# Kernel tuning notes

Measured on AMD Instinct MI355X. Metric: run time of the kernel, lower is better.

## Reference

```python
import jax, jax.numpy as jnp
import numpy as np

B, C, NS, NT = 8, 256, 16384, 2048
KQ = 64            # self-attention key/query dim
D = 64             # cond_conv_feat_dim
W0, W1, W2 = D * D, D * D, D * 1   # dynamic weight sizes (predict_mask=True)
B0, B1, B2 = D, D, 1
CTRL = W0 + W1 + W2 + B0 + B1 + B2  # 8385


def setup_inputs() -> dict:
    key = jax.random.key(0)
    ks = jax.random.split(key, 9)
    return {
        "scene_feat": jax.random.normal(ks[0], (B, C, NS), jnp.float32),
        "template_feat": jax.random.normal(ks[1], (B, C, NT), jnp.float32),
        # SelfAttention 1x1-conv (= linear over channels) weights
        "q_w": jax.random.normal(ks[2], (KQ, C), jnp.float32) * 0.02,
        "k_w": jax.random.normal(ks[3], (KQ, C), jnp.float32) * 0.02,
        "v_w": jax.random.normal(ks[4], (C, C), jnp.float32) * 0.02,
        # projection head of SimpleAggregator: Conv1d(3*C -> D, k=1) + ReLU
        "proj_w": jax.random.normal(ks[5], (D, 3 * C), jnp.float32) * 0.02,
        "proj_b": jnp.zeros((D,), jnp.float32),
        # controller head: Linear(C -> CTRL), init normal(std=0.01), bias 0
        "ctrl_w": jax.random.normal(ks[6], (CTRL, C), jnp.float32) * 0.01,
        "ctrl_b": jnp.zeros((CTRL,), jnp.float32),
    }


def _self_attention(x, q_w, k_w, v_w):
    # x: [B, C, N] -> [B, C_out, N]
    q = jnp.einsum("kc,bcn->bnk", q_w, x)          # [B, N, KQ]
    k = jnp.einsum("kc,bcn->bkn", k_w, x)          # [B, KQ, N]
    v = jnp.einsum("oc,bcn->bno", v_w, x)          # [B, N, C_out]
    attn = jax.nn.softmax(jnp.einsum("bnk,bkm->bnm", q / jnp.sqrt(jnp.float32(KQ)), k), axis=-1)
    y = jnp.einsum("bnm,bmo->bon", attn, v)        # [B, C_out, N]
    return y


def reference(scene_feat, template_feat, q_w, k_w, v_w, proj_w, proj_b, ctrl_w, ctrl_b):
    # ---- SimpleAggregator (self-attention on template inside) ----
    t_sa = _self_attention(template_feat, q_w, k_w, v_w)       # [B, C, NT]
    t_max = jnp.max(t_sa, axis=-1, keepdims=True)              # [B, C, 1]
    aggr = jnp.concatenate(
        [scene_feat - t_max, scene_feat * t_max, scene_feat], axis=1
    )                                                          # [B, 3C, NS]
    x = jax.nn.relu(jnp.einsum("oc,bcn->bon", proj_w, aggr) + proj_b[None, :, None])  # [B, D, NS]

    # ---- controller head on ORIGINAL template_feat max-pooled ----
    pooled = jnp.max(template_feat, axis=-1)                   # [B, C]
    params = pooled @ ctrl_w.T + ctrl_b                        # [B, CTRL]

    # parse_dynamic_params: splits = weights then biases
    o = 0
    w0 = params[:, o:o + W0].reshape(B, D, D); o += W0
    w1 = params[:, o:o + W1].reshape(B, D, D); o += W1
    w2 = params[:, o:o + W2].reshape(B, 1, D); o += W2
    b0 = params[:, o:o + B0]; o += B0
    b1 = params[:, o:o + B1]; o += B1
    b2 = params[:, o:o + B2]

    # per-sample dynamic 1x1 convs (groups=batch trick == batched GEMM)
    x = jax.nn.relu(jnp.einsum("boi,bin->bon", w0, x) + b0[:, :, None])
    x = jax.nn.relu(jnp.einsum("boi,bin->bon", w1, x) + b1[:, :, None])
    x = jnp.einsum("boi,bin->bon", w2, x) + b2[:, :, None]    # [B, 1, NS], no relu (mask layer)
    return x.reshape(B, NS)
```

## Files before the change

kernel.cpp:

```cpp
#include <hip/hip_runtime.h>


typedef __attribute__((ext_vector_type(8))) short short8;
typedef __attribute__((ext_vector_type(4))) short short4v;
typedef __attribute__((ext_vector_type(4))) float f32x4;

__device__ __forceinline__ unsigned short f2bf(float f){
  unsigned u = __float_as_uint(f);
  u += 0x7FFFu + ((u >> 16) & 1u);
  return (unsigned short)(u >> 16);
}
__device__ __forceinline__ unsigned fenc(float f){
  unsigned u = __float_as_uint(f);
  return (u & 0x80000000u) ? ~u : (u | 0x80000000u);
}
__device__ __forceinline__ float fdec(unsigned k){
  unsigned u = (k & 0x80000000u) ? (k & 0x7FFFFFFFu) : ~k;
  return __uint_as_float(u);
}

__global__ __launch_bounds__(256) void k0w(const float* __restrict__ qw,
    const float* __restrict__ kw, const float* __restrict__ vw,
    unsigned short* __restrict__ Wbf, unsigned* __restrict__ tmaxe,
    unsigned* __restrict__ pooledEnc){
  if (blockIdx.x == 0){
    const unsigned ninf = fenc(-3.0e38f);
    for (int i = threadIdx.x; i < 2048; i += 256){
      tmaxe[i] = 0u;
      pooledEnc[i] = ninf;
    }
  }
  const int e = (blockIdx.x * 256 + threadIdx.x) * 4;
  const int row = e >> 8, c = e & 255;
  const float* src;
  float scl = 1.0f;
  if (row < 64){ src = qw + row * 256 + c; scl = 0.125f; }
  else if (row < 128){ src = kw + (row - 64) * 256 + c; }
  else { src = vw + (row - 128) * 256 + c; }
  float4 v = *(const float4*)src;
  short4v o;
  o[0] = (short)f2bf(v.x * scl); o[1] = (short)f2bf(v.y * scl);
  o[2] = (short)f2bf(v.z * scl); o[3] = (short)f2bf(v.w * scl);
  *(short4v*)(Wbf + e) = o;
}

__global__ __launch_bounds__(256) void k0_tt(const float* __restrict__ T,
    unsigned short* __restrict__ Tt, unsigned* __restrict__ pooledEnc){
  const int b = blockIdx.x, nt = blockIdx.y, ct = blockIdx.z;
  const int n0 = nt * 128, c0 = ct * 32;
  const int tid = threadIdx.x;
  __shared__ float Ls[32][129];
  const int cr = tid >> 3, nq = tid & 7;
  const float* src = T + ((size_t)b * 256 + c0 + cr) * 2048 + n0 + nq * 16;
  float4 v0 = ((const float4*)src)[0];
  float4 v1 = ((const float4*)src)[1];
  float4 v2 = ((const float4*)src)[2];
  float4 v3 = ((const float4*)src)[3];
  float mx = fmaxf(fmaxf(fmaxf(v0.x, v0.y), fmaxf(v0.z, v0.w)),
                   fmaxf(fmaxf(v1.x, v1.y), fmaxf(v1.z, v1.w)));
  mx = fmaxf(mx, fmaxf(fmaxf(fmaxf(v2.x, v2.y), fmaxf(v2.z, v2.w)),
                       fmaxf(fmaxf(v3.x, v3.y), fmaxf(v3.z, v3.w))));
  mx = fmaxf(mx, __shfl_xor(mx, 1));
  mx = fmaxf(mx, __shfl_xor(mx, 2));
  mx = fmaxf(mx, __shfl_xor(mx, 4));
  if (nq == 0) atomicMax(&pooledEnc[b * 256 + c0 + cr], fenc(mx));
  float* lr = &Ls[cr][nq * 16];
  *(float4*)lr = v0; *(float4*)(lr + 4) = v1;
  *(float4*)(lr + 8) = v2; *(float4*)(lr + 12) = v3;
  __syncthreads();
  const int nr = tid >> 1, ch = tid & 1;
  unsigned short ob[16];
  #pragma unroll
  for (int j = 0; j < 16; j++) ob[j] = f2bf(Ls[ch * 16 + j][nr]);
  unsigned short* dst = Tt + ((size_t)b * 2048 + n0 + nr) * 256 + c0 + ch * 16;
  *(short8*)dst = *(short8*)&ob[0];
  *(short8*)(dst + 8) = *(short8*)&ob[8];
}

__global__ __launch_bounds__(256) void k23_qkv_params(
    const unsigned short* __restrict__ Wbf, const unsigned short* __restrict__ Tt,
    unsigned short* __restrict__ qo, unsigned short* __restrict__ ko,
    unsigned short* __restrict__ vt,
    const unsigned* __restrict__ pooledEnc, const float* __restrict__ cw,
    const float* __restrict__ cb, float* __restrict__ params){
  const int wg = blockIdx.x;
  const int tid = threadIdx.x, lane = tid & 63, w = tid >> 6;
  if (wg >= 512){
    __shared__ float P[8 * 256];
    for (int i = tid; i < 2048; i += 256) P[i] = fdec(pooledEnc[i]);
    __syncthreads();
    const int r = (wg - 512) * 4 + w;
    if (r >= 8385) return;
    float4 c4 = ((const float4*)(cw + (size_t)r * 256))[lane];
    float bias = cb[r];
    #pragma unroll
    for (int b = 0; b < 8; b++){
      const float* pbp = P + b * 256 + lane * 4;
      float s = c4.x * pbp[0] + c4.y * pbp[1] + c4.z * pbp[2] + c4.w * pbp[3];
      #pragma unroll
      for (int d = 1; d < 64; d <<= 1) s += __shfl_xor(s, d);
      if (lane == 0) params[b * 8385 + r] = s + bias;
    }
    return;
  }
  const int b = wg & 7, nt = wg >> 3;
  const int n0 = nt * 32;
  const int l15 = lane & 15, g = lane >> 4;
  const unsigned short* Tb = Tt + (size_t)b * 2048 * 256;

  f32x4 aqk[2][2], av[4][2];
  #pragma unroll
  for (int i = 0; i < 2; i++)
    #pragma unroll
    for (int nf = 0; nf < 2; nf++) aqk[i][nf] = (f32x4){0.f,0.f,0.f,0.f};
  #pragma unroll
  for (int j = 0; j < 4; j++)
    #pragma unroll
    for (int nf = 0; nf < 2; nf++) av[j][nf] = (f32x4){0.f,0.f,0.f,0.f};

  #pragma unroll 2
  for (int kc = 0; kc < 8; kc++){
    short8 bfr[2];
    #pragma unroll
    for (int nf = 0; nf < 2; nf++)
      bfr[nf] = *(const short8*)(Tb + (size_t)(n0 + nf * 16 + l15) * 256 + kc * 32 + g * 8);
    short8 aq[2];
    #pragma unroll
    for (int i = 0; i < 2; i++)
      aq[i] = *(const short8*)(Wbf + (size_t)((2 * w + i) * 16 + l15) * 256 + kc * 32 + g * 8);
    short8 afv[4];
    #pragma unroll
    for (int j = 0; j < 4; j++)
      afv[j] = *(const short8*)(Wbf + (size_t)(128 + (4 * w + j) * 16 + l15) * 256 + kc * 32 + g * 8);
    #pragma unroll
    for (int i = 0; i < 2; i++)
      #pragma unroll
      for (int nf = 0; nf < 2; nf++)
        aqk[i][nf] = __builtin_amdgcn_mfma_f32_16x16x32_bf16(aq[i], bfr[nf], aqk[i][nf], 0, 0, 0);
    #pragma unroll
    for (int j = 0; j < 4; j++)
      #pragma unroll
      for (int nf = 0; nf < 2; nf++)
        av[j][nf] = __builtin_amdgcn_mfma_f32_16x16x32_bf16(bfr[nf], afv[j], av[j][nf], 0, 0, 0);
  }
  unsigned short* qk = (w < 2) ? qo : ko;
  #pragma unroll
  for (int i = 0; i < 2; i++)
    #pragma unroll
    for (int nf = 0; nf < 2; nf++){
      int n = n0 + nf * 16 + l15;
      int cbase = (w & 1) * 32 + i * 16 + g * 4;
      short4v pk;
      #pragma unroll
      for (int r = 0; r < 4; r++) pk[r] = (short)f2bf(aqk[i][nf][r]);
      *(short4v*)(qk + ((size_t)b * 2048 + n) * 64 + cbase) = pk;
    }
  #pragma unroll
  for (int j = 0; j < 4; j++)
    #pragma unroll
    for (int nf = 0; nf < 2; nf++){
      int o = (4 * w + j) * 16 + l15;
      int nb2 = n0 + nf * 16 + g * 4;
      short4v pv;
      #pragma unroll
      for (int r = 0; r < 4; r++) pv[r] = (short)f2bf(av[j][nf][r]);
      *(short4v*)(vt + ((size_t)b * 256 + o) * 2048 + nb2) = pv;
    }
}

__global__ __launch_bounds__(512, 4) void kA_scores(
    const unsigned short* __restrict__ Qg, const unsigned short* __restrict__ Kg,
    unsigned short* __restrict__ Pg, float* __restrict__ sbuf,
    int b0, int bshift){
  const int wg = blockIdx.x;
  const int bmask = (1 << bshift) - 1;
  const int b = b0 + (wg & bmask);
  const int q0 = (wg >> bshift) * 32;
  const int qb0 = (wg >> bshift) * 2;
  const int tid = threadIdx.x, lane = tid & 63, w = tid >> 6;
  const int l15 = lane & 15, g = lane >> 4;
  __shared__ float wsum[32][8];
  const unsigned short* Qb = Qg + (size_t)b * 2048 * 64;
  const unsigned short* Kb = Kg + (size_t)b * 2048 * 64;
  unsigned short* Pb = Pg + (size_t)(wg & bmask) * 2048 * 2048;

  short8 qf[2][2];
  #pragma unroll
  for (int qi = 0; qi < 2; qi++)
    #pragma unroll
    for (int kc = 0; kc < 2; kc++)
      qf[qi][kc] = *(const short8*)(Qb + (size_t)(q0 + qi * 16 + l15) * 64 + kc * 32 + g * 8);

  float ps[2][4];
  #pragma unroll
  for (int qi = 0; qi < 2; qi++)
    #pragma unroll
    for (int r = 0; r < 4; r++) ps[qi][r] = 0.f;

  const int wm0 = w * 256;
  #pragma unroll
  for (int mt = 0; mt < 4; ++mt){
    const int mb = wm0 + mt * 64;
    short8 kf[4][2];
    #pragma unroll
    for (int mi = 0; mi < 4; mi++)
      #pragma unroll
      for (int kc = 0; kc < 2; kc++)
        kf[mi][kc] = *(const short8*)(Kb + (size_t)(mb + mi * 16 + l15) * 64 + kc * 32 + g * 8);
    #pragma unroll
    for (int qi = 0; qi < 2; qi++){
      f32x4 sa[4];
      #pragma unroll
      for (int mi = 0; mi < 4; mi++) sa[mi] = (f32x4){0.f,0.f,0.f,0.f};
      #pragma unroll
      for (int mi = 0; mi < 4; mi++)
        #pragma unroll
        for (int kc = 0; kc < 2; kc++)
          sa[mi] = __builtin_amdgcn_mfma_f32_16x16x32_bf16(qf[qi][kc], kf[mi][kc], sa[mi], 0, 0, 0);
      #pragma unroll
      for (int mi = 0; mi < 4; mi++){
        short4v pk;
        #pragma unroll
        for (int r = 0; r < 4; r++){
          float p = __expf(sa[mi][r]);
          ps[qi][r] += p;
          pk[r] = (short)f2bf(p);
        }
        *(short4v*)(Pb + ((size_t)((qb0 + qi) * 128 + w * 16 + mt * 4 + mi)) * 256 + lane * 4) = pk;
      }
    }
  }
  #pragma unroll
  for (int qi = 0; qi < 2; qi++)
    #pragma unroll
    for (int r = 0; r < 4; r++){
      float t = ps[qi][r];
      t += __shfl_xor(t, 1); t += __shfl_xor(t, 2);
      t += __shfl_xor(t, 4); t += __shfl_xor(t, 8);
      if (l15 == 0) wsum[qi * 16 + g * 4 + r][w] = t;
    }
  __syncthreads();
  if (tid < 32){
    float t = 0.f;
    #pragma unroll
    for (int i = 0; i < 8; i++) t += wsum[tid][i];
    sbuf[(size_t)b * 2048 + q0 + tid] = t;
  }
}

__global__ __launch_bounds__(256, 2) void kB_pv(
    const unsigned short* __restrict__ Pg, const unsigned short* __restrict__ Vt,
    const float* __restrict__ sbuf, unsigned* __restrict__ tmaxe,
    int b0, int bshift){
  const int wg = blockIdx.x;
  const int bmask = (1 << bshift) - 1;
  const int b = b0 + (wg & bmask);
  const int rest = wg >> bshift;
  const int oh = rest & 1;
  const int n0 = (rest >> 1) * 64;
  const int qb0 = n0 >> 4;
  const int tid = threadIdx.x, lane = tid & 63, w = tid >> 6;
  const int l15 = lane & 15, g = lane >> 4;
  __shared__ __align__(16) unsigned char smem[2][24576];

  const unsigned short* Pb = Pg + (size_t)(wg & bmask) * 2048 * 2048;
  const unsigned short* Vb = Vt + ((size_t)b * 256 + oh * 128) * 2048;

  f32x4 acc[4][2];
  #pragma unroll
  for (int ni = 0; ni < 4; ni++)
    #pragma unroll
    for (int oi = 0; oi < 2; oi++) acc[ni][oi] = (f32x4){0.f,0.f,0.f,0.f};

  short8 stg[6];
  auto LOADS = [&](int m0){
    const int mb0 = m0 >> 4;
    #pragma unroll
    for (int k = 0; k < 6; k++){
      int d = k * 4096 + tid * 16;
      if (k < 2){
        int ti = d >> 9;
        int qi = ti >> 2, mi = ti & 3;
        stg[k] = *(const short8*)(Pb + ((size_t)(qb0 + qi) * 128 + mb0 + mi) * 256 + ((d & 511) >> 1));
      } else {
        int dv = d - 8192;
        int row = dv >> 7;
        stg[k] = *(const short8*)(Vb + (size_t)row * 2048 + m0 + ((dv & 127) >> 1));
      }
    }
  };
  auto WRITES = [&](unsigned char* buf){
    #pragma unroll
    for (int k = 0; k < 6; k++){
      int d = k * 4096 + tid * 16;
      if (k < 2){
        int ti = d >> 9;
        int qi = ti >> 2, mi = ti & 3;
        int lane0 = (d & 511) >> 3;
        #pragma unroll
        for (int idx = 0; idx < 8; idx++){
          int Lp = lane0 + (idx >> 2), r = idx & 3;
          int row = qi * 16 + ((Lp >> 4) << 2) + r;
          int col = mi * 16 + (Lp & 15);
          *(unsigned short*)(buf + ((row * 128 + col * 2) ^ ((row & 7) << 4))) =
              ((const unsigned short*)&stg[k])[idx];
        }
      } else {
        int dv = d - 8192;
        int row = dv >> 7;
        *(short8*)(buf + 8192 + (dv ^ ((row & 7) << 4))) = stg[k];
      }
    }
  };

  LOADS(0);
  WRITES(smem[0]);
  __syncthreads();

  for (int t = 0; t < 32; ++t){
    unsigned char* cur = smem[t & 1];
    if (t < 31) LOADS((t + 1) * 64);
    short8 af[4][2], bf[2][2];
    #pragma unroll
    for (int ni = 0; ni < 4; ni++)
      #pragma unroll
      for (int kc = 0; kc < 2; kc++){
        int row = ni * 16 + l15;
        af[ni][kc] = *(const short8*)(cur + ((row * 128 + kc * 64 + g * 16) ^ ((row & 7) << 4)));
      }
    #pragma unroll
    for (int oi = 0; oi < 2; oi++)
      #pragma unroll
      for (int kc = 0; kc < 2; kc++){
        int row = w * 32 + oi * 16 + l15;
        bf[oi][kc] = *(const short8*)(cur + 8192 + ((row * 128 + kc * 64 + g * 16) ^ ((row & 7) << 4)));
      }
    #pragma unroll
    for (int ni = 0; ni < 4; ni++)
      #pragma unroll
      for (int oi = 0; oi < 2; oi++)
        #pragma unroll
        for (int kc = 0; kc < 2; kc++)
          acc[ni][oi] = __builtin_amdgcn_mfma_f32_16x16x32_bf16(af[ni][kc], bf[oi][kc], acc[ni][oi], 0, 0, 0);
    if (t < 31){
      WRITES(smem[(t + 1) & 1]);
      __syncthreads();
    }
  }
  float inv[4][4];
  #pragma unroll
  for (int ni = 0; ni < 4; ni++)
    #pragma unroll
    for (int r = 0; r < 4; r++)
      inv[ni][r] = 1.0f / sbuf[(size_t)b * 2048 + n0 + ni * 16 + g * 4 + r];
  #pragma unroll
  for (int oi = 0; oi < 2; oi++){
    float cm = -1e30f;
    #pragma unroll
    for (int ni = 0; ni < 4; ni++)
      #pragma unroll
      for (int r = 0; r < 4; r++)
        cm = fmaxf(cm, acc[ni][oi][r] * inv[ni][r]);
    cm = fmaxf(cm, __shfl_xor(cm, 16));
    cm = fmaxf(cm, __shfl_xor(cm, 32));
    if (lane < 16)
      atomicMax(&tmaxe[b * 256 + oh * 128 + w * 32 + oi * 16 + lane], fenc(cm));
  }
}

__global__ __launch_bounds__(256) void k5_weff(const float* __restrict__ proj_w,
    const float* __restrict__ proj_b, const unsigned* __restrict__ tmaxe,
    const float* __restrict__ params, unsigned short* __restrict__ weff,
    float* __restrict__ beff, unsigned short* __restrict__ w0b,
    unsigned short* __restrict__ w1b){
  const int b = blockIdx.y, o = blockIdx.x;
  const int c = threadIdx.x;
  float t = fdec(tmaxe[b * 256 + c]);
  float p0 = proj_w[o * 768 + c];
  float p1 = proj_w[o * 768 + 256 + c];
  float p2 = proj_w[o * 768 + 512 + c];
  weff[((size_t)b * 64 + o) * 256 + c] = f2bf(p0 + p1 * t + p2);
  float s = p0 * t;
  #pragma unroll
  for (int d = 1; d < 64; d <<= 1) s += __shfl_xor(s, d);
  __shared__ float sm[4];
  if ((c & 63) == 0) sm[c >> 6] = s;
  __syncthreads();
  if (c == 0) beff[b * 64 + o] = proj_b[o] - (sm[0] + sm[1] + sm[2] + sm[3]);
  if (c < 64)        w0b[((size_t)b * 64 + o) * 64 + c] = f2bf(params[b * 8385 + o * 64 + c]);
  else if (c < 128)  w1b[((size_t)b * 64 + o) * 64 + (c - 64)] = f2bf(params[b * 8385 + 4096 + o * 64 + (c - 64)]);
}

__global__ __launch_bounds__(512) void k6_main(const float* __restrict__ Sg,
    const unsigned short* __restrict__ weff, const float* __restrict__ beff,
    const unsigned short* __restrict__ w0b, const unsigned short* __restrict__ w1b,
    const float* __restrict__ params, float* __restrict__ out){
  const int b = blockIdx.y, nt = blockIdx.x;
  const int n0 = nt * 256;
  const int tid = threadIdx.x, lane = tid & 63, w = tid >> 6;
  const int l15 = lane & 15, g = lane >> 4;
  __shared__ __align__(16) unsigned char smem[65536];
  unsigned short* H0 = (unsigned short*)smem;
  unsigned char*  Ub = smem + 32768;
  unsigned short* H1 = (unsigned short*)Ub;

  const float* Sb = Sg + (size_t)b * 256 * 16384;
  const unsigned short* We = weff + (size_t)b * 64 * 256;
  f32x4 a0[4][2];
  #pragma unroll
  for (int mi = 0; mi < 4; mi++)
    #pragma unroll
    for (int ni = 0; ni < 2; ni++) a0[mi][ni] = (f32x4){0.f,0.f,0.f,0.f};

  const int scc = tid & 31;
  const int snb = (tid >> 5) * 16;
  for (int k0 = 0; k0 < 256; k0 += 32){
    const float* src = Sb + (size_t)(k0 + scc) * 16384 + n0 + snb;
    float4 v0 = ((const float4*)src)[0];
    float4 v1 = ((const float4*)src)[1];
    float4 v2 = ((const float4*)src)[2];
    float4 v3 = ((const float4*)src)[3];
    float vals[16] = {v0.x,v0.y,v0.z,v0.w, v1.x,v1.y,v1.z,v1.w,
                      v2.x,v2.y,v2.z,v2.w, v3.x,v3.y,v3.z,v3.w};
    #pragma unroll
    for (int j = 0; j < 16; j++){
      int n = snb + j;
      unsigned byteo = ((unsigned)(n * 64 + scc * 2)) ^ ((unsigned)((n >> 1) & 3) << 4);
      *(unsigned short*)(Ub + byteo) = f2bf(vals[j]);
    }
    __syncthreads();
    short8 bf0[2];
    #pragma unroll
    for (int ni = 0; ni < 2; ni++){
      int n = w * 32 + ni * 16 + l15;
      bf0[ni] = *(const short8*)(Ub + (((unsigned)(n * 64 + g * 16)) ^ ((unsigned)((n >> 1) & 3) << 4)));
    }
    #pragma unroll
    for (int mi = 0; mi < 4; mi++){
      short8 af = *(const short8*)(We + (mi * 16 + l15) * 256 + k0 + g * 8);
      #pragma unroll
      for (int ni = 0; ni < 2; ni++)
        a0[mi][ni] = __builtin_amdgcn_mfma_f32_16x16x32_bf16(af, bf0[ni], a0[mi][ni], 0, 0, 0);
    }
    __syncthreads();
  }
  const float* be = beff + b * 64;
  #pragma unroll
  for (int mi = 0; mi < 4; mi++)
    #pragma unroll
    for (int ni = 0; ni < 2; ni++){
      int n = w * 32 + ni * 16 + l15;
      unsigned base = ((unsigned)(n * 128 + mi * 32 + g * 8)) ^ ((unsigned)((n & 7) << 4));
      unsigned short hh[4];
      #pragma unroll
      for (int r = 0; r < 4; r++){
        int o = mi * 16 + g * 4 + r;
        hh[r] = f2bf(fmaxf(a0[mi][ni][r] + be[o], 0.f));
      }
      *(unsigned*)((unsigned char*)H0 + base)     = (unsigned)hh[0] | ((unsigned)hh[1] << 16);
      *(unsigned*)((unsigned char*)H0 + base + 4) = (unsigned)hh[2] | ((unsigned)hh[3] << 16);
    }
  __syncthreads();
  f32x4 a1[4][2];
  #pragma unroll
  for (int mi = 0; mi < 4; mi++)
    #pragma unroll
    for (int ni = 0; ni < 2; ni++) a1[mi][ni] = (f32x4){0.f,0.f,0.f,0.f};
  const unsigned short* W0 = w0b + (size_t)b * 4096;
  #pragma unroll
  for (int ks = 0; ks < 2; ks++){
    short8 bfh[2];
    #pragma unroll
    for (int ni = 0; ni < 2; ni++){
      int n = w * 32 + ni * 16 + l15;
      unsigned off = ((unsigned)(n * 128 + ks * 64 + g * 16)) ^ ((unsigned)((n & 7) << 4));
      bfh[ni] = *(const short8*)((unsigned char*)H0 + off);
    }
    #pragma unroll
    for (int mi = 0; mi < 4; mi++){
      short8 af = *(const short8*)(W0 + (mi * 16 + l15) * 64 + ks * 32 + g * 8);
      #pragma unroll
      for (int ni = 0; ni < 2; ni++)
        a1[mi][ni] = __builtin_amdgcn_mfma_f32_16x16x32_bf16(af, bfh[ni], a1[mi][ni], 0, 0, 0);
    }
  }
  const float* pp = params + (size_t)b * 8385;
  const float* b0p = pp + 8256;
  #pragma unroll
  for (int mi = 0; mi < 4; mi++)
    #pragma unroll
    for (int ni = 0; ni < 2; ni++){
      int n = w * 32 + ni * 16 + l15;
      unsigned base = ((unsigned)(n * 128 + mi * 32 + g * 8)) ^ ((unsigned)((n & 7) << 4));
      unsigned short hh[4];
      #pragma unroll
      for (int r = 0; r < 4; r++){
        int o = mi * 16 + g * 4 + r;
        hh[r] = f2bf(fmaxf(a1[mi][ni][r] + b0p[o], 0.f));
      }
      *(unsigned*)((unsigned char*)H1 + base)     = (unsigned)hh[0] | ((unsigned)hh[1] << 16);
      *(unsigned*)((unsigned char*)H1 + base + 4) = (unsigned)hh[2] | ((unsigned)hh[3] << 16);
    }
  __syncthreads();
  f32x4 a2[4][2];
  #pragma unroll
  for (int mi = 0; mi < 4; mi++)
    #pragma unroll
    for (int ni = 0; ni < 2; ni++) a2[mi][ni] = (f32x4){0.f,0.f,0.f,0.f};
  const unsigned short* W1 = w1b + (size_t)b * 4096;
  #pragma unroll
  for (int ks = 0; ks < 2; ks++){
    short8 bfh[2];
    #pragma unroll
    for (int ni = 0; ni < 2; ni++){
      int n = w * 32 + ni * 16 + l15;
      unsigned off = ((unsigned)(n * 128 + ks * 64 + g * 16)) ^ ((unsigned)((n & 7) << 4));
      bfh[ni] = *(const short8*)((unsigned char*)H1 + off);
    }
    #pragma unroll
    for (int mi = 0; mi < 4; mi++){
      short8 af = *(const short8*)(W1 + (mi * 16 + l15) * 64 + ks * 32 + g * 8);
      #pragma unroll
      for (int ni = 0; ni < 2; ni++)
        a2[mi][ni] = __builtin_amdgcn_mfma_f32_16x16x32_bf16(af, bfh[ni], a2[mi][ni], 0, 0, 0);
    }
  }
  const float* b1p = pp + 8320;
  const float* w2p = pp + 8192;
  float b2v = pp[8384];
  #pragma unroll
  for (int ni = 0; ni < 2; ni++){
    float t = 0.f;
    #pragma unroll
    for (int mi = 0; mi < 4; mi++)
      #pragma unroll
      for (int r = 0; r < 4; r++){
        int o = mi * 16 + g * 4 + r;
        t += w2p[o] * fmaxf(a2[mi][ni][r] + b1p[o], 0.f);
      }
    t += __shfl_xor(t, 16);
    t += __shfl_xor(t, 32);
    if (lane < 16)
      out[(size_t)b * 16384 + n0 + w * 32 + ni * 16 + l15] = t + b2v;
  }
}

extern "C" void kernel_launch(void* const* d_in, const int* in_sizes, int n_in,
                              void* d_out, int out_size, void* d_ws, size_t ws_size,
                              hipStream_t stream){
  const float* scene = (const float*)d_in[0];
  const float* tmpl  = (const float*)d_in[1];
  const float* qw    = (const float*)d_in[2];
  const float* kw    = (const float*)d_in[3];
  const float* vw    = (const float*)d_in[4];
  const float* pw    = (const float*)d_in[5];
  const float* pb    = (const float*)d_in[6];
  const float* cw    = (const float*)d_in[7];
  const float* cb    = (const float*)d_in[8];
  float* out = (float*)d_out;
  char* ws = (char*)d_ws;

  unsigned short* Q      = (unsigned short*)(ws + 0);
  unsigned short* K      = (unsigned short*)(ws + (2u << 20));
  unsigned short* V      = (unsigned short*)(ws + (4u << 20));
  unsigned*       pooledEnc = (unsigned*)(ws + (12u << 20));
  unsigned*       tmaxe  = (unsigned*)(ws + (12u << 20) + 8192);
  float*          params = (float*)(ws + (12u << 20) + 16384);
  unsigned short* w0b    = (unsigned short*)(ws + (13u << 20));
  unsigned short* w1b    = (unsigned short*)(ws + (13u << 20) + 65536);
  unsigned short* weff   = (unsigned short*)(ws + (13u << 20) + 131072);
  float*          beff   = (float*)(ws + (13u << 20) + 131072 + 262144);
  float*          sbuf   = (float*)(ws + (14u << 20));
  unsigned short* Wbf    = (unsigned short*)(ws + (14u << 20) + 131072);
  unsigned short* Pbuf   = (unsigned short*)(ws + (16u << 20));
  unsigned short* Tt     = Pbuf;

  const size_t pPerBatch = (size_t)2048 * 2048 * 2;
  size_t avail = ws_size > (16u << 20) ? ws_size - (16u << 20) : 0;
  int nb = 8, bshift = 3;
  while (nb > 1 && (size_t)nb * pPerBatch > avail){ nb >>= 1; bshift--; }

  k0w<<<dim3(96), dim3(256), 0, stream>>>(qw, kw, vw, Wbf, tmaxe, pooledEnc);
  k0_tt<<<dim3(8, 16, 8), dim3(256), 0, stream>>>(tmpl, Tt, pooledEnc);
  k23_qkv_params<<<dim3(512 + 2097), dim3(256), 0, stream>>>(Wbf, Tt, Q, K, V,
                                                             pooledEnc, cw, cb, params);
  for (int b0 = 0; b0 < 8; b0 += nb){
    kA_scores<<<dim3(64 * nb), dim3(512), 0, stream>>>(Q, K, Pbuf, sbuf, b0, bshift);
    kB_pv<<<dim3(64 * nb), dim3(256), 0, stream>>>(Pbuf, V, sbuf, tmaxe, b0, bshift);
  }
  k5_weff<<<dim3(64, 8), dim3(256), 0, stream>>>(pw, pb, tmaxe, params, weff, beff, w0b, w1b);
  k6_main<<<dim3(64, 8), dim3(512), 0, stream>>>(scene, weff, beff, w0b, w1b, params, out);
}
```

Before: 151.5 us.

## Store P row-major via swapped MFMA operands, prefetch scene tiles, raise kB occupancy

The score kernel swaps the MFMA A/B operands so each lane holds a row of P. P can then be written in plain row-major layout, and row sums reduce across lane groups instead of within 16 lanes. The PV kernel now loads P tiles with simple coalesced rows and writes them to LDS as whole 16-byte vectors, replacing eight scalar scattered LDS stores per load. The final scene-projection kernel also software-prefetches the next k-chunk of scene features into registers, and kB_pv's launch bound minimum occupancy rises from 2 to 3, which may constrain registers.

```diff
diff --git a/kernel.cpp b/kernel.cpp
--- a/kernel.cpp
+++ b/kernel.cpp
@@ -176,7 +176,6 @@
   const int bmask = (1 << bshift) - 1;
   const int b = b0 + (wg & bmask);
   const int q0 = (wg >> bshift) * 32;
-  const int qb0 = (wg >> bshift) * 2;
   const int tid = threadIdx.x, lane = tid & 63, w = tid >> 6;
   const int l15 = lane & 15, g = lane >> 4;
   __shared__ float wsum[32][8];
@@ -191,11 +190,7 @@
     for (int kc = 0; kc < 2; kc++)
       qf[qi][kc] = *(const short8*)(Qb + (size_t)(q0 + qi * 16 + l15) * 64 + kc * 32 + g * 8);
 
-  float ps[2][4];
-  #pragma unroll
-  for (int qi = 0; qi < 2; qi++)
-    #pragma unroll
-    for (int r = 0; r < 4; r++) ps[qi][r] = 0.f;
+  float ps[2] = {0.f, 0.f};
 
   const int wm0 = w * 256;
   #pragma unroll
@@ -216,29 +211,27 @@
       for (int mi = 0; mi < 4; mi++)
         #pragma unroll
         for (int kc = 0; kc < 2; kc++)
-          sa[mi] = __builtin_amdgcn_mfma_f32_16x16x32_bf16(qf[qi][kc], kf[mi][kc], sa[mi], 0, 0, 0);
+          sa[mi] = __builtin_amdgcn_mfma_f32_16x16x32_bf16(kf[mi][kc], qf[qi][kc], sa[mi], 0, 0, 0);
       #pragma unroll
       for (int mi = 0; mi < 4; mi++){
         short4v pk;
         #pragma unroll
         for (int r = 0; r < 4; r++){
           float p = __expf(sa[mi][r]);
-          ps[qi][r] += p;
+          ps[qi] += p;
           pk[r] = (short)f2bf(p);
         }
-        *(short4v*)(Pb + ((size_t)((qb0 + qi) * 128 + w * 16 + mt * 4 + mi)) * 256 + lane * 4) = pk;
-      }
-    }
-  }
-  #pragma unroll
-  for (int qi = 0; qi < 2; qi++)
-    #pragma unroll
-    for (int r = 0; r < 4; r++){
-      float t = ps[qi][r];
-      t += __shfl_xor(t, 1); t += __shfl_xor(t, 2);
-      t += __shfl_xor(t, 4); t += __shfl_xor(t, 8);
-      if (l15 == 0) wsum[qi * 16 + g * 4 + r][w] = t;
-    }
+        *(short4v*)(Pb + (size_t)(q0 + qi * 16 + l15) * 2048 + mb + mi * 16 + g * 4) = pk;
+      }
+    }
+  }
+  #pragma unroll
+  for (int qi = 0; qi < 2; qi++){
+    float t = ps[qi];
+    t += __shfl_xor(t, 16);
+    t += __shfl_xor(t, 32);
+    if (lane < 16) wsum[qi * 16 + l15][w] = t;
+  }
   __syncthreads();
   if (tid < 32){
     float t = 0.f;
@@ -248,7 +241,7 @@
   }
 }
 
-__global__ __launch_bounds__(256, 2) void kB_pv(
+__global__ __launch_bounds__(256, 3) void kB_pv(
     const unsigned short* __restrict__ Pg, const unsigned short* __restrict__ Vt,
     const float* __restrict__ sbuf, unsigned* __restrict__ tmaxe,
     int b0, int bshift){
@@ -258,7 +251,6 @@
   const int rest = wg >> bshift;
   const int oh = rest & 1;
   const int n0 = (rest >> 1) * 64;
-  const int qb0 = n0 >> 4;
   const int tid = threadIdx.x, lane = tid & 63, w = tid >> 6;
   const int l15 = lane & 15, g = lane >> 4;
   __shared__ __align__(16) unsigned char smem[2][24576];
@@ -274,14 +266,12 @@
 
   short8 stg[6];
   auto LOADS = [&](int m0){
-    const int mb0 = m0 >> 4;
     #pragma unroll
     for (int k = 0; k < 6; k++){
       int d = k * 4096 + tid * 16;
       if (k < 2){
-        int ti = d >> 9;
-        int qi = ti >> 2, mi = ti & 3;
-        stg[k] = *(const short8*)(Pb + ((size_t)(qb0 + qi) * 128 + mb0 + mi) * 256 + ((d & 511) >> 1));
+        int row = d >> 7;
+        stg[k] = *(const short8*)(Pb + (size_t)(n0 + row) * 2048 + m0 + ((d & 127) >> 1));
       } else {
         int dv = d - 8192;
         int row = dv >> 7;
@@ -294,17 +284,8 @@
     for (int k = 0; k < 6; k++){
       int d = k * 4096 + tid * 16;
       if (k < 2){
-        int ti = d >> 9;
-        int qi = ti >> 2, mi = ti & 3;
-        int lane0 = (d & 511) >> 3;
-        #pragma unroll
-        for (int idx = 0; idx < 8; idx++){
-          int Lp = lane0 + (idx >> 2), r = idx & 3;
-          int row = qi * 16 + ((Lp >> 4) << 2) + r;
-          int col = mi * 16 + (Lp & 15);
-          *(unsigned short*)(buf + ((row * 128 + col * 2) ^ ((row & 7) << 4))) =
-              ((const unsigned short*)&stg[k])[idx];
-        }
+        int row = d >> 7;
+        *(short8*)(buf + (d ^ ((row & 7) << 4))) = stg[k];
       } else {
         int dv = d - 8192;
         int row = dv >> 7;
@@ -414,12 +395,12 @@
 
   const int scc = tid & 31;
   const int snb = (tid >> 5) * 16;
+  const float* src0 = Sb + (size_t)scc * 16384 + n0 + snb;
+  float4 v0 = ((const float4*)src0)[0];
+  float4 v1 = ((const float4*)src0)[1];
+  float4 v2 = ((const float4*)src0)[2];
+  float4 v3 = ((const float4*)src0)[3];
   for (int k0 = 0; k0 < 256; k0 += 32){
-    const float* src = Sb + (size_t)(k0 + scc) * 16384 + n0 + snb;
-    float4 v0 = ((const float4*)src)[0];
-    float4 v1 = ((const float4*)src)[1];
-    float4 v2 = ((const float4*)src)[2];
-    float4 v3 = ((const float4*)src)[3];
     float vals[16] = {v0.x,v0.y,v0.z,v0.w, v1.x,v1.y,v1.z,v1.w,
                       v2.x,v2.y,v2.z,v2.w, v3.x,v3.y,v3.z,v3.w};
     #pragma unroll
@@ -427,6 +408,13 @@
       int n = snb + j;
       unsigned byteo = ((unsigned)(n * 64 + scc * 2)) ^ ((unsigned)((n >> 1) & 3) << 4);
       *(unsigned short*)(Ub + byteo) = f2bf(vals[j]);
+    }
+    if (k0 < 224){
+      const float* nsrc = Sb + (size_t)(k0 + 32 + scc) * 16384 + n0 + snb;
+      v0 = ((const float4*)nsrc)[0];
+      v1 = ((const float4*)nsrc)[1];
+      v2 = ((const float4*)nsrc)[2];
+      v3 = ((const float4*)nsrc)[3];
     }
     __syncthreads();
     short8 bf0[2];
```

Result: faster. 144.6 us (-4.6%).
